# Kernel tuning notes

Measured on AMD Instinct MI355X. Metric: run time of the kernel, lower is better.

The kernel has to match this reference:

```python
import jax, jax.numpy as jnp
import numpy as np


def setup_inputs() -> dict:
    key = jax.random.key(0)
    kq, kk, kv = jax.random.split(key, 3)
    B, S, D = 4, 4096, 64
    q = jax.random.normal(kq, (B, S, D), dtype=jnp.float32)
    k = jax.random.normal(kk, (B, S, D), dtype=jnp.float32)
    v = jax.random.normal(kv, (B, S, D), dtype=jnp.float32)
    return {"q": q, "k": k, "v": v}


def reference(q, k, v):
    # Faithful math of the original blocked loop:
    #   output_i += exp(Q_i @ K_j^T) @ V_j, summed over all column blocks j
    # which is exactly unnormalized exponential attention:
    #   out = exp(Q K^T) V  (no 1/sqrt(d) scaling, no softmax normalization,
    #   no max-subtraction -- matching the source module's math).
    scores = jnp.einsum("bqd,bkd->bqk", q, k)  # [B, Sq, Sk]
    return jnp.einsum("bqk,bkd->bqd", jnp.exp(scores), v)  # [B, Sq, D]
```

## Files before the change

### kernel.cpp

```cpp
#include <hip/hip_runtime.h>
#include <hip/hip_bf16.h>


typedef short    s16x4 __attribute__((ext_vector_type(4)));
typedef short    s16x8 __attribute__((ext_vector_type(8)));
typedef _Float16 h16x8 __attribute__((ext_vector_type(8)));
typedef float    fx4   __attribute__((ext_vector_type(4)));
typedef float    fx16  __attribute__((ext_vector_type(16)));

constexpr int S = 4096, D = 64, BN = 128;
constexpr int TILES = S / BN;
constexpr int TILE_SHORTS  = 16 * 512;
constexpr int BATCH_SHORTS = TILES * TILE_SHORTS;

__device__ __forceinline__ unsigned short f2bf(float x) {
    unsigned u = __float_as_uint(x);
    u = (u + 0x7FFFu + ((u >> 16) & 1u)) >> 16;
    return (unsigned short)u;
}
__device__ __forceinline__ float bf2f(unsigned short h) {
    return __uint_as_float(((unsigned)h) << 16);
}
__device__ __forceinline__ unsigned short f2h(float x) {
    union { _Float16 h; unsigned short s; } u;
    u.h = (_Float16)x;
    return u.s;
}
__device__ __forceinline__ unsigned pack_bf16(float lo, float hi) {
    __hip_bfloat162 r = __float22bfloat162_rn(make_float2(lo, hi));
    union { __hip_bfloat162 b; unsigned u; } c;
    c.b = r;
    return c.u;
}
__device__ __forceinline__ h16x8 as_h16(s16x8 x) {
    union { s16x8 s; h16x8 h; } u;
    u.s = x;
    return u.h;
}

__global__ __launch_bounds__(256) void prep2(
    const float* __restrict__ k, const float* __restrict__ v,
    unsigned short* __restrict__ kf, unsigned short* __restrict__ vf)
{
    __shared__ unsigned short tile[128 * 72];
    const int tid   = threadIdx.x;
    const int which = blockIdx.x & 1;
    const int t     = (blockIdx.x >> 1) & 31;
    const int b     = blockIdx.x >> 6;
    const float* src = (which ? v : k) + ((size_t)b * S + t * BN) * D;

    #pragma unroll
    for (int i = 0; i < 8; ++i) {
        int f   = i * 256 + tid;
        int row = f >> 4;
        int c4  = (f & 15) << 2;
        float4 x = *(const float4*)(src + row * D + c4);
        s16x4 o;
        if (which) o = (s16x4){(short)f2bf(x.x), (short)f2bf(x.y),
                               (short)f2bf(x.z), (short)f2bf(x.w)};
        else       o = (s16x4){(short)f2h(x.x), (short)f2h(x.y),
                               (short)f2h(x.z), (short)f2h(x.w)};
        *(s16x4*)&tile[row * 72 + c4] = o;
    }
    __syncthreads();

    const int lane = tid & 63;
    unsigned short* dst = (which ? vf : kf) + (size_t)b * BATCH_SHORTS + t * TILE_SHORTS;
    #pragma unroll
    for (int i = 0; i < 4; ++i) {
        int c = (tid >> 6) * 4 + i;
        s16x8 o;
        if (which == 0) {
            int row = (c >> 2) * 32 + (lane & 31);
            int dc  = (c & 3) * 16 + (lane >> 5) * 8;
            o = *(const s16x8*)&tile[row * 72 + dc];
        } else {
            int r0 = (c >> 1) * 16 + (lane >> 5) * 8;
            int dc = (c & 1) * 32 + (lane & 31);
            #pragma unroll
            for (int j = 0; j < 8; ++j) o[j] = (short)tile[(r0 + j) * 72 + dc];
        }
        *(s16x8*)(dst + c * 512 + lane * 8) = o;
    }
}

__global__ __launch_bounds__(512, 2) void attn_stream(
    const float* __restrict__ q, const unsigned short* __restrict__ kf,
    const unsigned short* __restrict__ vf, float* __restrict__ out)
{
    __shared__ float scratch[6 * 2048];

    const int tid = threadIdx.x, lane = tid & 63, w = tid >> 6;
    const int h = lane >> 5, m5 = lane & 31;
    const int mt = w & 1, kkq = w >> 1;
    const int b = blockIdx.y, q0 = blockIdx.x * 64;

    const unsigned short* kq = kf + (size_t)b * BATCH_SHORTS + (kkq * 4) * 512 + lane * 8;
    const unsigned short* vq = vf + (size_t)b * BATCH_SHORTS + (kkq * 4) * 512 + lane * 8;

    h16x8 qf[4];
    {
        const float* qrow = q + ((size_t)b * S + q0 + mt * 32 + m5) * D + h * 8;
        #pragma unroll
        for (int ks = 0; ks < 4; ++ks) {
            float4 a = *(const float4*)(qrow + ks * 16);
            float4 c = *(const float4*)(qrow + ks * 16 + 4);
            qf[ks] = (h16x8){(_Float16)a.x, (_Float16)a.y, (_Float16)a.z, (_Float16)a.w,
                             (_Float16)c.x, (_Float16)c.y, (_Float16)c.z, (_Float16)c.w};
        }
    }

    fx16 oacc[2] = {};

    s16x8 ka[4], va[4], kb[4], vb[4];

    auto ldfrag = [&](int t, s16x8* kd, s16x8* vd) {
        const size_t off = (size_t)t * TILE_SHORTS;
        #pragma unroll
        for (int i = 0; i < 4; ++i) {
            kd[i] = *(const s16x8*)(kq + off + i * 512);
            vd[i] = *(const s16x8*)(vq + off + i * 512);
        }
    };

    auto compute = [&](const s16x8* kc, const s16x8* vc) {
        fx16 sa = {};
        #pragma unroll
        for (int ks = 0; ks < 4; ++ks)
            sa = __builtin_amdgcn_mfma_f32_32x32x16_f16(as_h16(kc[ks]), qf[ks], sa, 0, 0, 0);

        unsigned p01[8];
        #pragma unroll
        for (int rp = 0; rp < 8; ++rp)
            p01[rp] = pack_bf16(__expf(sa[2 * rp]), __expf(sa[2 * rp + 1]));

        union frag { unsigned u[4]; s16x8 v; };
        frag A[2];
#if __has_builtin(__builtin_amdgcn_permlane32_swap)
        typedef unsigned uix2 __attribute__((ext_vector_type(2)));
        uix2 r0 = __builtin_amdgcn_permlane32_swap(p01[0], p01[2], false, false);
        uix2 r1 = __builtin_amdgcn_permlane32_swap(p01[1], p01[3], false, false);
        A[0].u[0] = r0.x; A[0].u[1] = r1.x; A[0].u[2] = r0.y; A[0].u[3] = r1.y;
        uix2 r2 = __builtin_amdgcn_permlane32_swap(p01[4], p01[6], false, false);
        uix2 r3 = __builtin_amdgcn_permlane32_swap(p01[5], p01[7], false, false);
        A[1].u[0] = r2.x; A[1].u[1] = r3.x; A[1].u[2] = r2.y; A[1].u[3] = r3.y;
#else
        unsigned sw[8];
        #pragma unroll
        for (int rp = 0; rp < 8; ++rp)
            sw[rp] = (unsigned)__shfl_xor((int)p01[rp], 32, 64);
        A[0].u[0] = h ? sw[2]   : p01[0];
        A[0].u[1] = h ? sw[3]   : p01[1];
        A[0].u[2] = h ? p01[2]  : sw[0];
        A[0].u[3] = h ? p01[3]  : sw[1];
        A[1].u[0] = h ? sw[6]   : p01[4];
        A[1].u[1] = h ? sw[7]   : p01[5];
        A[1].u[2] = h ? p01[6]  : sw[4];
        A[1].u[3] = h ? p01[7]  : sw[5];
#endif

        #pragma unroll
        for (int u = 0; u < 2; ++u)
            #pragma unroll
            for (int dt = 0; dt < 2; ++dt)
                oacc[dt] = __builtin_amdgcn_mfma_f32_32x32x16_bf16(
                    A[u].v, vc[u * 2 + dt], oacc[dt], 0, 0, 0);
    };

    ldfrag(0, ka, va);
    #pragma unroll 1
    for (int t = 0; t < TILES; t += 2) {
        ldfrag(t + 1, kb, vb);
        compute(ka, va);
        ldfrag((t + 2) & (TILES - 1), ka, va);
        compute(kb, vb);
    }

    if (kkq > 0) {
        float* dst = scratch + (size_t)(mt * 3 + (kkq - 1)) * 2048;
        #pragma unroll
        for (int dt = 0; dt < 2; ++dt)
            #pragma unroll
            for (int r = 0; r < 16; ++r)
                dst[(dt * 16 + r) * 64 + lane] = oacc[dt][r];
    }
    __syncthreads();
    if (kkq == 0) {
        float* ob = out + (size_t)b * S * D;
        #pragma unroll
        for (int dt = 0; dt < 2; ++dt)
            #pragma unroll
            for (int r = 0; r < 16; ++r) {
                float val = oacc[dt][r];
                #pragma unroll
                for (int p = 0; p < 3; ++p)
                    val += scratch[(size_t)(mt * 3 + p) * 2048 + (dt * 16 + r) * 64 + lane];
                int row = q0 + mt * 32 + (r & 3) + 8 * (r >> 2) + 4 * h;
                ob[(size_t)row * D + dt * 32 + m5] = val;
            }
    }
}

__global__ __launch_bounds__(1024) void attn_fallback(
    const float* __restrict__ q, const float* __restrict__ k,
    const float* __restrict__ v, float* __restrict__ out)
{
    __shared__ unsigned short Kh[64][72];
    __shared__ unsigned short Kl[64][72];
    __shared__ unsigned short Vt[64][68];
    __shared__ unsigned short Pf[64][72];

    const int tid = threadIdx.x, lane = tid & 63, wave = tid >> 6;
    const int quad = lane >> 4, tq = lane & 15;
    const int kkb = wave & 3, mba = wave >> 2;
    const int b = blockIdx.y, q0 = blockIdx.x * 64;
    const float* qb = q + (size_t)b * S * D;
    const float* kb = k + (size_t)b * S * D;
    const float* vb = v + (size_t)b * S * D;
    float* ob = out + (size_t)b * S * D;

    s16x8 qh[2], ql[2];
    {
        const float* qrow = qb + (size_t)(q0 + mba * 16 + tq) * D;
        #pragma unroll
        for (int ks = 0; ks < 2; ++ks) {
            const float* src = qrow + ks * 32 + quad * 8;
            float4 f0 = *(const float4*)src;
            float4 f1 = *(const float4*)(src + 4);
            float f[8] = {f0.x, f0.y, f0.z, f0.w, f1.x, f1.y, f1.z, f1.w};
            #pragma unroll
            for (int j = 0; j < 8; ++j) {
                unsigned short hh = f2bf(f[j]);
                qh[ks][j] = (short)hh;
                ql[ks][j] = (short)f2bf(f[j] - bf2f(hh));
            }
        }
    }
    fx4 oacc = {0.f, 0.f, 0.f, 0.f};
    const int krow = tid >> 4, kc4 = (tid & 15) << 2;
    const int vd = tid & 63, vk = (tid >> 6) << 2;

    for (int t = 0; t < S / 64; ++t) {
        __syncthreads();
        const float* kt = kb + (size_t)(t * 64 + krow) * D;
        const float* vt = vb + (size_t)(t * 64 + vk) * D;
        {
            float4 kv = *(const float4*)(kt + kc4);
            unsigned short h0 = f2bf(kv.x), h1 = f2bf(kv.y), h2 = f2bf(kv.z), h3 = f2bf(kv.w);
            s16x4 a = {(short)h0, (short)h1, (short)h2, (short)h3};
            s16x4 l4 = {(short)f2bf(kv.x - bf2f(h0)), (short)f2bf(kv.y - bf2f(h1)),
                        (short)f2bf(kv.z - bf2f(h2)), (short)f2bf(kv.w - bf2f(h3))};
            *(s16x4*)&Kh[krow][kc4] = a;
            *(s16x4*)&Kl[krow][kc4] = l4;
            const float* vs = vt + vd;
            s16x4 vv = {(short)f2bf(vs[0]), (short)f2bf(vs[D]),
                        (short)f2bf(vs[2 * D]), (short)f2bf(vs[3 * D])};
            *(s16x4*)&Vt[vd][vk] = vv;
        }
        __syncthreads();
        fx4 sacc = {0.f, 0.f, 0.f, 0.f};
        #pragma unroll
        for (int ks = 0; ks < 2; ++ks) {
            s16x8 kah = *(const s16x8*)&Kh[kkb * 16 + tq][ks * 32 + quad * 8];
            s16x8 kal = *(const s16x8*)&Kl[kkb * 16 + tq][ks * 32 + quad * 8];
            sacc = __builtin_amdgcn_mfma_f32_16x16x32_bf16(kah, qh[ks], sacc, 0, 0, 0);
            sacc = __builtin_amdgcn_mfma_f32_16x16x32_bf16(kah, ql[ks], sacc, 0, 0, 0);
            sacc = __builtin_amdgcn_mfma_f32_16x16x32_bf16(kal, qh[ks], sacc, 0, 0, 0);
        }
        s16x4 pp = {(short)f2bf(__expf(sacc[0])), (short)f2bf(__expf(sacc[1])),
                    (short)f2bf(__expf(sacc[2])), (short)f2bf(__expf(sacc[3]))};
        *(s16x4*)&Pf[mba * 16 + tq][kkb * 16 + (quad << 2)] = pp;
        __syncthreads();
        #pragma unroll
        for (int ks = 0; ks < 2; ++ks) {
            s16x8 pa = *(const s16x8*)&Pf[mba * 16 + tq][ks * 32 + quad * 8];
            const unsigned short* vr = &Vt[kkb * 16 + tq][ks * 32 + quad * 8];
            s16x4 va = *(const s16x4*)vr;
            s16x4 vb2 = *(const s16x4*)(vr + 4);
            s16x8 vfull = __builtin_shufflevector(va, vb2, 0, 1, 2, 3, 4, 5, 6, 7);
            oacc = __builtin_amdgcn_mfma_f32_16x16x32_bf16(pa, vfull, oacc, 0, 0, 0);
        }
    }
    #pragma unroll
    for (int r = 0; r < 4; ++r)
        ob[(size_t)(q0 + mba * 16 + quad * 4 + r) * D + kkb * 16 + tq] = oacc[r];
}

extern "C" void kernel_launch(void* const* d_in, const int* in_sizes, int n_in,
                              void* d_out, int out_size, void* d_ws, size_t ws_size,
                              hipStream_t stream) {
    const float* q = (const float*)d_in[0];
    const float* k = (const float*)d_in[1];
    const float* v = (const float*)d_in[2];
    float* out = (float*)d_out;
    const int nbatch = in_sizes[0] / (S * D);
    const size_t elems = (size_t)nbatch * S * D;

    const size_t need = elems * 2 * 2;
    if (nbatch == 4 && ws_size >= need && d_ws != nullptr) {
        unsigned short* kf = (unsigned short*)d_ws;
        unsigned short* vf = kf + elems;

        prep2<<<nbatch * TILES * 2, 256, 0, stream>>>(k, v, kf, vf);
        dim3 grid(S / 64, nbatch);
        attn_stream<<<grid, 512, 0, stream>>>(q, kf, vf, out);
    } else {
        dim3 grid(S / 64, nbatch);
        attn_fallback<<<grid, 1024, 0, stream>>>(q, k, v, out);
    }
}
```

Measured before the change: 94.38 us.

## Fuse K/V conversion into attention kernel with split-K partials and reduction

```diff
diff --git a/kernel.cpp b/kernel.cpp
--- a/kernel.cpp
+++ b/kernel.cpp
@@ -8,10 +8,9 @@
 typedef float    fx4   __attribute__((ext_vector_type(4)));
 typedef float    fx16  __attribute__((ext_vector_type(16)));
 
-constexpr int S = 4096, D = 64, BN = 128;
-constexpr int TILES = S / BN;
-constexpr int TILE_SHORTS  = 16 * 512;
-constexpr int BATCH_SHORTS = TILES * TILE_SHORTS;
+constexpr int S = 4096, D = 64, BQ = 64, BN = 64;
+constexpr int KH = 4;
+constexpr int NT = S / BN / KH;
 
 __device__ __forceinline__ unsigned short f2bf(float x) {
     unsigned u = __float_as_uint(x);
@@ -32,71 +31,22 @@
     c.b = r;
     return c.u;
 }
-__device__ __forceinline__ h16x8 as_h16(s16x8 x) {
-    union { s16x8 s; h16x8 h; } u;
-    u.s = x;
-    return u.h;
-}
-
-__global__ __launch_bounds__(256) void prep2(
-    const float* __restrict__ k, const float* __restrict__ v,
-    unsigned short* __restrict__ kf, unsigned short* __restrict__ vf)
+
+__global__ __launch_bounds__(256, 4) void attn_fused(
+    const float* __restrict__ q, const float* __restrict__ k,
+    const float* __restrict__ v, float* __restrict__ partial)
 {
-    __shared__ unsigned short tile[128 * 72];
-    const int tid   = threadIdx.x;
-    const int which = blockIdx.x & 1;
-    const int t     = (blockIdx.x >> 1) & 31;
-    const int b     = blockIdx.x >> 6;
-    const float* src = (which ? v : k) + ((size_t)b * S + t * BN) * D;
-
-    #pragma unroll
-    for (int i = 0; i < 8; ++i) {
-        int f   = i * 256 + tid;
-        int row = f >> 4;
-        int c4  = (f & 15) << 2;
-        float4 x = *(const float4*)(src + row * D + c4);
-        s16x4 o;
-        if (which) o = (s16x4){(short)f2bf(x.x), (short)f2bf(x.y),
-                               (short)f2bf(x.z), (short)f2bf(x.w)};
-        else       o = (s16x4){(short)f2h(x.x), (short)f2h(x.y),
-                               (short)f2h(x.z), (short)f2h(x.w)};
-        *(s16x4*)&tile[row * 72 + c4] = o;
-    }
-    __syncthreads();
-
-    const int lane = tid & 63;
-    unsigned short* dst = (which ? vf : kf) + (size_t)b * BATCH_SHORTS + t * TILE_SHORTS;
-    #pragma unroll
-    for (int i = 0; i < 4; ++i) {
-        int c = (tid >> 6) * 4 + i;
-        s16x8 o;
-        if (which == 0) {
-            int row = (c >> 2) * 32 + (lane & 31);
-            int dc  = (c & 3) * 16 + (lane >> 5) * 8;
-            o = *(const s16x8*)&tile[row * 72 + dc];
-        } else {
-            int r0 = (c >> 1) * 16 + (lane >> 5) * 8;
-            int dc = (c & 1) * 32 + (lane & 31);
-            #pragma unroll
-            for (int j = 0; j < 8; ++j) o[j] = (short)tile[(r0 + j) * 72 + dc];
-        }
-        *(s16x8*)(dst + c * 512 + lane * 8) = o;
-    }
-}
-
-__global__ __launch_bounds__(512, 2) void attn_stream(
-    const float* __restrict__ q, const unsigned short* __restrict__ kf,
-    const unsigned short* __restrict__ vf, float* __restrict__ out)
-{
-    __shared__ float scratch[6 * 2048];
+    __shared__ unsigned short Ks[64 * 72];
+    __shared__ unsigned short Vt[64 * 72];
+    __shared__ float red[4096];
 
     const int tid = threadIdx.x, lane = tid & 63, w = tid >> 6;
     const int h = lane >> 5, m5 = lane & 31;
-    const int mt = w & 1, kkq = w >> 1;
-    const int b = blockIdx.y, q0 = blockIdx.x * 64;
-
-    const unsigned short* kq = kf + (size_t)b * BATCH_SHORTS + (kkq * 4) * 512 + lane * 8;
-    const unsigned short* vq = vf + (size_t)b * BATCH_SHORTS + (kkq * 4) * 512 + lane * 8;
+    const int mt = w & 1, kkh = w >> 1;
+    const int b = blockIdx.y, q0 = blockIdx.x * BQ, kh = blockIdx.z;
+
+    const float* kbase = k + ((size_t)b * S + (size_t)kh * NT * BN) * D;
+    const float* vbase = v + ((size_t)b * S + (size_t)kh * NT * BN) * D;
 
     h16x8 qf[4];
     {
@@ -110,24 +60,56 @@
         }
     }
 
+    const int krow0 = tid >> 4;
+    const int kc4   = (tid & 15) << 2;
+    const int vd    = tid & 63;
+    const int vg    = w;
+
+    float4 kraw[4];
+    float  vraw[16];
+
+    auto load_raw = [&](int t) {
+        const float* kt = kbase + (size_t)t * BN * D;
+        const float* vt = vbase + (size_t)t * BN * D;
+        #pragma unroll
+        for (int i = 0; i < 4; ++i)
+            kraw[i] = *(const float4*)(kt + (i * 16 + krow0) * D + kc4);
+        #pragma unroll
+        for (int j = 0; j < 16; ++j)
+            vraw[j] = vt[(vg * 16 + j) * D + vd];
+    };
+
+    auto cvt_store = [&]() {
+        #pragma unroll
+        for (int i = 0; i < 4; ++i) {
+            s16x4 o = {(short)f2h(kraw[i].x), (short)f2h(kraw[i].y),
+                       (short)f2h(kraw[i].z), (short)f2h(kraw[i].w)};
+            *(s16x4*)&Ks[(i * 16 + krow0) * 72 + kc4] = o;
+        }
+        union { unsigned u[4]; s16x8 v; } p0, p1;
+        #pragma unroll
+        for (int jj = 0; jj < 4; ++jj) {
+            p0.u[jj] = pack_bf16(vraw[2 * jj],     vraw[2 * jj + 1]);
+            p1.u[jj] = pack_bf16(vraw[8 + 2 * jj], vraw[9 + 2 * jj]);
+        }
+        *(s16x8*)&Vt[vd * 72 + vg * 16]     = p0.v;
+        *(s16x8*)&Vt[vd * 72 + vg * 16 + 8] = p1.v;
+    };
+
     fx16 oacc[2] = {};
 
-    s16x8 ka[4], va[4], kb[4], vb[4];
-
-    auto ldfrag = [&](int t, s16x8* kd, s16x8* vd) {
-        const size_t off = (size_t)t * TILE_SHORTS;
-        #pragma unroll
-        for (int i = 0; i < 4; ++i) {
-            kd[i] = *(const s16x8*)(kq + off + i * 512);
-            vd[i] = *(const s16x8*)(vq + off + i * 512);
-        }
-    };
-
-    auto compute = [&](const s16x8* kc, const s16x8* vc) {
+    load_raw(0);
+    for (int t = 0; t < NT; ++t) {
+        cvt_store();
+        __syncthreads();
+        if (t + 1 < NT) load_raw(t + 1);
+
         fx16 sa = {};
         #pragma unroll
-        for (int ks = 0; ks < 4; ++ks)
-            sa = __builtin_amdgcn_mfma_f32_32x32x16_f16(as_h16(kc[ks]), qf[ks], sa, 0, 0, 0);
+        for (int ks = 0; ks < 4; ++ks) {
+            h16x8 a = *(const h16x8*)&Ks[(kkh * 32 + m5) * 72 + ks * 16 + h * 8];
+            sa = __builtin_amdgcn_mfma_f32_32x32x16_f16(a, qf[ks], sa, 0, 0, 0);
+        }
 
         unsigned p01[8];
         #pragma unroll
@@ -149,55 +131,59 @@
         #pragma unroll
         for (int rp = 0; rp < 8; ++rp)
             sw[rp] = (unsigned)__shfl_xor((int)p01[rp], 32, 64);
-        A[0].u[0] = h ? sw[2]   : p01[0];
-        A[0].u[1] = h ? sw[3]   : p01[1];
-        A[0].u[2] = h ? p01[2]  : sw[0];
-        A[0].u[3] = h ? p01[3]  : sw[1];
-        A[1].u[0] = h ? sw[6]   : p01[4];
-        A[1].u[1] = h ? sw[7]   : p01[5];
-        A[1].u[2] = h ? p01[6]  : sw[4];
-        A[1].u[3] = h ? p01[7]  : sw[5];
+        A[0].u[0] = h ? sw[2]  : p01[0];
+        A[0].u[1] = h ? sw[3]  : p01[1];
+        A[0].u[2] = h ? p01[2] : sw[0];
+        A[0].u[3] = h ? p01[3] : sw[1];
+        A[1].u[0] = h ? sw[6]  : p01[4];
+        A[1].u[1] = h ? sw[7]  : p01[5];
+        A[1].u[2] = h ? p01[6] : sw[4];
+        A[1].u[3] = h ? p01[7] : sw[5];
 #endif
 
         #pragma unroll
-        for (int u = 0; u < 2; ++u)
-            #pragma unroll
-            for (int dt = 0; dt < 2; ++dt)
+        for (int ss = 0; ss < 2; ++ss)
+            #pragma unroll
+            for (int dt = 0; dt < 2; ++dt) {
+                s16x8 vv = *(const s16x8*)&Vt[(dt * 32 + m5) * 72
+                                              + kkh * 32 + ss * 16 + h * 8];
                 oacc[dt] = __builtin_amdgcn_mfma_f32_32x32x16_bf16(
-                    A[u].v, vc[u * 2 + dt], oacc[dt], 0, 0, 0);
-    };
-
-    ldfrag(0, ka, va);
-    #pragma unroll 1
-    for (int t = 0; t < TILES; t += 2) {
-        ldfrag(t + 1, kb, vb);
-        compute(ka, va);
-        ldfrag((t + 2) & (TILES - 1), ka, va);
-        compute(kb, vb);
-    }
-
-    if (kkq > 0) {
-        float* dst = scratch + (size_t)(mt * 3 + (kkq - 1)) * 2048;
+                    A[ss].v, vv, oacc[dt], 0, 0, 0);
+            }
+
+        __syncthreads();
+    }
+
+    if (kkh == 1) {
         #pragma unroll
         for (int dt = 0; dt < 2; ++dt)
             #pragma unroll
             for (int r = 0; r < 16; ++r)
-                dst[(dt * 16 + r) * 64 + lane] = oacc[dt][r];
+                red[((mt * 2 + dt) * 16 + r) * 64 + lane] = oacc[dt][r];
     }
     __syncthreads();
-    if (kkq == 0) {
-        float* ob = out + (size_t)b * S * D;
+    if (kkh == 0) {
+        float* pout = partial + ((size_t)kh * 4 + b) * S * D;
         #pragma unroll
         for (int dt = 0; dt < 2; ++dt)
             #pragma unroll
             for (int r = 0; r < 16; ++r) {
-                float val = oacc[dt][r];
-                #pragma unroll
-                for (int p = 0; p < 3; ++p)
-                    val += scratch[(size_t)(mt * 3 + p) * 2048 + (dt * 16 + r) * 64 + lane];
+                float val = oacc[dt][r] + red[((mt * 2 + dt) * 16 + r) * 64 + lane];
                 int row = q0 + mt * 32 + (r & 3) + 8 * (r >> 2) + 4 * h;
-                ob[(size_t)row * D + dt * 32 + m5] = val;
+                pout[(size_t)row * D + dt * 32 + m5] = val;
             }
+    }
+}
+
+__global__ __launch_bounds__(256) void reduce4(
+    const float4* __restrict__ p, float4* __restrict__ o, int n4, int stride4)
+{
+    int i = blockIdx.x * 256 + threadIdx.x;
+    if (i < n4) {
+        float4 a = p[i], b = p[i + stride4],
+               c = p[i + 2 * stride4], d = p[i + 3 * stride4];
+        o[i] = make_float4(a.x + b.x + c.x + d.x, a.y + b.y + c.y + d.y,
+                           a.z + b.z + c.z + d.z, a.w + b.w + c.w + d.w);
     }
 }
 
@@ -207,7 +193,7 @@
 {
     __shared__ unsigned short Kh[64][72];
     __shared__ unsigned short Kl[64][72];
-    __shared__ unsigned short Vt[64][68];
+    __shared__ unsigned short Vs[64][68];
     __shared__ unsigned short Pf[64][72];
 
     const int tid = threadIdx.x, lane = tid & 63, wave = tid >> 6;
@@ -255,7 +241,7 @@
             const float* vs = vt + vd;
             s16x4 vv = {(short)f2bf(vs[0]), (short)f2bf(vs[D]),
                         (short)f2bf(vs[2 * D]), (short)f2bf(vs[3 * D])};
-            *(s16x4*)&Vt[vd][vk] = vv;
+            *(s16x4*)&Vs[vd][vk] = vv;
         }
         __syncthreads();
         fx4 sacc = {0.f, 0.f, 0.f, 0.f};
@@ -274,7 +260,7 @@
         #pragma unroll
         for (int ks = 0; ks < 2; ++ks) {
             s16x8 pa = *(const s16x8*)&Pf[mba * 16 + tq][ks * 32 + quad * 8];
-            const unsigned short* vr = &Vt[kkb * 16 + tq][ks * 32 + quad * 8];
+            const unsigned short* vr = &Vs[kkb * 16 + tq][ks * 32 + quad * 8];
             s16x4 va = *(const s16x4*)vr;
             s16x4 vb2 = *(const s16x4*)(vr + 4);
             s16x8 vfull = __builtin_shufflevector(va, vb2, 0, 1, 2, 3, 4, 5, 6, 7);
@@ -296,14 +282,14 @@
     const int nbatch = in_sizes[0] / (S * D);
     const size_t elems = (size_t)nbatch * S * D;
 
-    const size_t need = elems * 2 * 2;
+    const size_t need = (size_t)KH * elems * 4;
     if (nbatch == 4 && ws_size >= need && d_ws != nullptr) {
-        unsigned short* kf = (unsigned short*)d_ws;
-        unsigned short* vf = kf + elems;
-
-        prep2<<<nbatch * TILES * 2, 256, 0, stream>>>(k, v, kf, vf);
-        dim3 grid(S / 64, nbatch);
-        attn_stream<<<grid, 512, 0, stream>>>(q, kf, vf, out);
+        float* partial = (float*)d_ws;
+        dim3 grid(S / BQ, nbatch, KH);
+        attn_fused<<<grid, 256, 0, stream>>>(q, k, v, partial);
+        const int n4 = (int)(elems / 4);
+        reduce4<<<(n4 + 255) / 256, 256, 0, stream>>>(
+            (const float4*)partial, (float4*)out, n4, n4);
     } else {
         dim3 grid(S / 64, nbatch);
         attn_fallback<<<grid, 1024, 0, stream>>>(q, k, v, out);
```

New measurement: 98.97 us. 1.05x slower.
